# Kernel tuning notes

Hardware: AMD Instinct MI355X
Metric: run time of the kernel (lower is better)

Reference implementation:

```python
import jax, jax.numpy as jnp
import numpy as np

H = 64   # hidden_size
N = 128  # input_size (num nodes)
B = 64   # batch
T = 96   # seq_len
LN_EPS = 1e-5


def setup_inputs() -> dict:
    key = jax.random.key(0)
    ks = jax.random.split(key, 4)
    x = jax.random.normal(ks[0], (B, T, N), jnp.float32)
    # xavier_uniform-like scale for per-node gate weights [N, 1+H, 4H]
    lim = float(np.sqrt(6.0 / ((1 + H) + 4 * H)))
    w = jax.random.uniform(ks[1], (N, 1 + H, 4 * H), jnp.float32, -lim, lim)
    b = jnp.zeros((N, 4 * H), jnp.float32)
    ln_g = jnp.ones((H,), jnp.float32)
    ln_b = jnp.zeros((H,), jnp.float32)
    fc_w = jax.random.normal(ks[2], (1, H), jnp.float32) * (1.0 / np.sqrt(H))
    fc_b = jnp.zeros((1,), jnp.float32)
    return {"x": x, "w": w, "b": b, "ln_g": ln_g, "ln_b": ln_b,
            "fc_w": fc_w, "fc_b": fc_b}


def _crelu(z):
    return jnp.maximum(z.real, 0) + 1j * jnp.maximum(z.imag, 0)


def _csigmoid(z):
    # torch.sigmoid on complex: 1/(1+exp(-z))
    return 1.0 / (1.0 + jnp.exp(-z))


def _fc_att(x, pool_axes):
    # adaptive_avg_pool to 1 over pool_axes, (C)ReLU, sigmoid, rescale
    squeeze = jnp.mean(x, axis=pool_axes, keepdims=True)
    if jnp.iscomplexobj(x):
        exc = _crelu(squeeze)
        return x * _csigmoid(exc)
    exc = jnp.maximum(squeeze, 0)
    return x * jax.nn.sigmoid(exc)


def reference(x, w, b, ln_g, ln_b, fc_w, fc_b):
    Bb, Tt, Nn = x.shape
    h0 = jnp.zeros((Bb, Nn, H), x.dtype)
    c0 = jnp.zeros((Bb, Nn, H), x.dtype)

    def step(carry, x_t):  # x_t: [B, N]
        h, c = carry
        comb = jnp.concatenate([x_t[..., None], h], axis=-1)      # [B,N,1+H]
        gates = jnp.einsum('bni,nio->bno', comb, w) + b            # [B,N,4H]
        i_g, f_g, o_g, c_tilda = jnp.split(gates, 4, axis=-1)
        # NOTE: original cell does NOT apply tanh to c_tilda
        c_new = jax.nn.sigmoid(f_g) * c + jax.nn.sigmoid(i_g) * c_tilda
        h_new = jax.nn.sigmoid(o_g) * jnp.tanh(c_new)
        return (h_new, c_new), h_new

    _, hs = jax.lax.scan(step, (h0, c0), jnp.swapaxes(x, 0, 1))    # [T,B,N,H]
    lstm_out = jnp.sum(hs, axis=0)                                  # sum over time -> [B,N,H]

    # inter_op: FFT pairwise interaction over the node axis
    m = jnp.fft.rfft(lstm_out, axis=1, norm='ortho')                # [B,F,H] complex, F=N//2+1
    x_f = m[:, :, None, :] * m[:, None, :, :]                       # [B,F,F,H]
    x_f = _fc_att(x_f, (2, 3))
    x_f = jnp.sum(x_f, axis=1)                                      # [B,F,H]
    n_out = 2 * (x_f.shape[1] - 1)                                  # torch irfft default n
    feats = jnp.fft.irfft(x_f, n=n_out, axis=1, norm='ortho')       # [B,N,H] real
    feats = _fc_att(feats, (2,))
    out = jnp.sum(feats, axis=1)                                    # [B,H]

    # LayerNorm(H) -> Linear(H,1) -> sigmoid
    mu = jnp.mean(out, axis=-1, keepdims=True)
    var = jnp.var(out, axis=-1, keepdims=True)
    out = (out - mu) / jnp.sqrt(var + LN_EPS) * ln_g + ln_b
    out = out @ fc_w.T + fc_b                                       # [B,1]
    return jax.nn.sigmoid(out)
```

## Files before the change

kernel.cpp:

```cpp
#include <hip/hip_runtime.h>
#include <math.h>

#define T_STEPS 96
#define N_NODES 128
#define B_SZ 64
#define H_SZ 64

typedef __attribute__((ext_vector_type(8))) __bf16 bf16x8;
typedef __attribute__((ext_vector_type(4))) float f32x4;

__device__ __forceinline__ float rcp_fast(float x){ return __builtin_amdgcn_rcpf(x); }
__device__ __forceinline__ float exp2_fast(float x){ return __builtin_amdgcn_exp2f(x); }
__device__ __forceinline__ float sigm(float v){ return rcp_fast(1.0f + __expf(-v)); }

__global__ __launch_bounds__(512, 2) void lstm_kernel(
    const float* __restrict__ x, const float* __restrict__ w,
    const float* __restrict__ bias, float* __restrict__ yout)
{
  __shared__ __align__(16) unsigned short hb[2][16*72];
  __shared__ float xsl[T_STEPS*16];

  const int n   = blockIdx.x >> 2;
  const int bq  = blockIdx.x & 3;
  const int tid = threadIdx.x;
  const int wv  = tid >> 6;
  const int ln  = tid & 63;
  const int l15 = ln & 15;
  const int q   = ln >> 4;

  for (int i = tid; i < 2*16*72; i += 512) ((unsigned short*)hb)[i] = 0;
  for (int i = tid; i < T_STEPS*16; i += 512){
    int t2 = i >> 4, bl = i & 15;
    xsl[i] = x[(bq*16 + bl)*(T_STEPS*N_NODES) + t2*N_NODES + n];
  }

  const float LOG2E = 1.4426950408889634f;
  const float* wn = w + n*(65*256);

  bf16x8 aF[2][2];
  f32x4 w0t[2], bgt[2];
#pragma unroll
  for (int t = 0; t < 2; ++t){
    const int gA  = l15 & 3;
    const float scA = (gA < 3) ? LOG2E : 1.0f;
    const int colA = gA*64 + wv*8 + t*4 + (l15 >> 2);
#pragma unroll
    for (int ks = 0; ks < 2; ++ks)
#pragma unroll
      for (int j = 0; j < 8; ++j)
        aF[t][ks][j] = (__bf16)(wn[(1 + ks*32 + q*8 + j)*256 + colA] * scA);
#pragma unroll
    for (int r = 0; r < 4; ++r){
      const float sc = (r < 3) ? LOG2E : 1.0f;
      const int colD = r*64 + wv*8 + t*4 + q;
      w0t[t][r] = wn[colD] * sc;
      bgt[t][r] = bias[n*256 + colD] * sc;
    }
  }

  float cv[2]  = {0.f, 0.f};
  float hsv[2] = {0.f, 0.f};
  __syncthreads();

#pragma unroll 2
  for (int t = 0; t < T_STEPS; ++t){
    const unsigned short* cur = hb[t & 1];
    unsigned short*       nxt = (unsigned short*)hb[(t & 1) ^ 1];

    bf16x8 b0 = *(const bf16x8*)&cur[l15*72 +  0 + q*8];
    bf16x8 b1 = *(const bf16x8*)&cur[l15*72 + 32 + q*8];
    float xv = xsl[t*16 + l15];

    f32x4 acc[2];
#pragma unroll
    for (int tl = 0; tl < 2; ++tl){
      f32x4 a = w0t[tl]*xv + bgt[tl];
      a = __builtin_amdgcn_mfma_f32_16x16x32_bf16(aF[tl][0], b0, a, 0,0,0);
      a = __builtin_amdgcn_mfma_f32_16x16x32_bf16(aF[tl][1], b1, a, 0,0,0);
      acc[tl] = a;
    }

#pragma unroll
    for (int tl = 0; tl < 2; ++tl){
      float gi = acc[tl][0], gf = acc[tl][1], go = acc[tl][2], ct = acc[tl][3];
      float ei = exp2_fast(-gi), ef = exp2_fast(-gf);
      float pf = 1.0f + ef, pi = 1.0f + ei;
      float num = fmaf(cv[tl], ei, cv[tl]);
      num = fmaf(ct, pf, num);
      float cn = num * rcp_fast(pf*pi);
      cv[tl] = cn;
      float eo = exp2_fast(-go);
      float ea = fminf(cn*2.8853900817779268f, 126.0f);
      float ec = exp2_fast(ea);
      float hn = (ec - 1.0f) * rcp_fast((1.0f + eo)*(ec + 1.0f));
      hsv[tl] += hn;
      nxt[l15*72 + wv*8 + tl*4 + q] =
          __builtin_bit_cast(unsigned short, (__bf16)hn);
    }
    __syncthreads();
  }

#pragma unroll
  for (int tl = 0; tl < 2; ++tl)
    yout[((bq*16 + l15)*N_NODES + n)*H_SZ + wv*8 + tl*4 + q] = hsv[tl];
}

__global__ __launch_bounds__(256, 2) void dft_kernel(
    const float* __restrict__ y, float* __restrict__ Mout)
{
  __shared__ __align__(16) float ysl[128*20];
  __shared__ float twc[128], tws[128];
  const int b   = blockIdx.x >> 2;
  const int hg  = blockIdx.x & 3;
  const int tid = threadIdx.x;

  if (tid < 128){
    float ang = (float)((double)tid * 0.04908738521234052);
    twc[tid] = cosf(ang);
    tws[tid] = sinf(ang);
  }
  for (int i = tid; i < 128*16; i += 256){
    int nn = i >> 4, h = i & 15;
    ysl[nn*20 + h] = y[(b*N_NODES + nn)*H_SZ + hg*16 + h];
  }
  __syncthreads();

  for (int o = tid; o < 65*4; o += 256){
    int k  = o >> 2;
    int hq = o & 3;
    float re0=0,re1=0,re2=0,re3=0,im0=0,im1=0,im2=0,im3=0;
    for (int nn = 0; nn < 128; ++nn){
      float4 yv = *(const float4*)&ysl[nn*20 + hq*4];
      int j = (k*nn) & 127;
      float cc = twc[j], ss = tws[j];
      re0 = fmaf(yv.x, cc, re0); im0 = fmaf(yv.x, -ss, im0);
      re1 = fmaf(yv.y, cc, re1); im1 = fmaf(yv.y, -ss, im1);
      re2 = fmaf(yv.z, cc, re2); im2 = fmaf(yv.z, -ss, im2);
      re3 = fmaf(yv.w, cc, re3); im3 = fmaf(yv.w, -ss, im3);
    }
    const float s = 0.08838834764831845f;
    const int hb2 = hg*16 + hq*4;
    float* mre = Mout + ((b*2+0)*65 + k)*H_SZ + hb2;
    float* mim = Mout + ((b*2+1)*65 + k)*H_SZ + hb2;
    mre[0]=re0*s; mre[1]=re1*s; mre[2]=re2*s; mre[3]=re3*s;
    mim[0]=im0*s; mim[1]=im1*s; mim[2]=im2*s; mim[3]=im3*s;
  }
}

__global__ __launch_bounds__(256, 1) void post_kernel(
    const float* __restrict__ y, const float* __restrict__ Mws,
    const float* __restrict__ ln_g, const float* __restrict__ ln_b,
    const float* __restrict__ fc_w, const float* __restrict__ fc_b,
    float* __restrict__ out)
{
  __shared__ float ysh[128*65];
  __shared__ float Mre[65*65];
  __shared__ float Mim[65*65];
  __shared__ float twc[128], tws[128];
  __shared__ float Sre[64], Sim[64];
  __shared__ float gr[65], gi[65];
  __shared__ float Gre[64], Gim[64];
  __shared__ float att[128];
  __shared__ float PQ[65*2], AA[65*2];
  __shared__ float outv[64];

  const int b   = blockIdx.x;
  const int tid = threadIdx.x;

  if (tid < 128){
    float ang = (float)((double)tid * 0.04908738521234052);
    twc[tid] = cosf(ang);
    tws[tid] = sinf(ang);
  }
  for (int i = tid; i < 128*16; i += 256){
    int nn = i >> 4, h4 = (i & 15)*4;
    float4 v = *(const float4*)&y[(b*N_NODES + nn)*H_SZ + h4];
    ysh[nn*65 + h4+0] = v.x; ysh[nn*65 + h4+1] = v.y;
    ysh[nn*65 + h4+2] = v.z; ysh[nn*65 + h4+3] = v.w;
  }
  for (int i = tid; i < 65*16; i += 256){
    int k = i >> 4, h4 = (i & 15)*4;
    float4 vr = *(const float4*)&Mws[((b*2+0)*65 + k)*H_SZ + h4];
    float4 vi = *(const float4*)&Mws[((b*2+1)*65 + k)*H_SZ + h4];
    Mre[k*65 + h4+0] = vr.x; Mre[k*65 + h4+1] = vr.y;
    Mre[k*65 + h4+2] = vr.z; Mre[k*65 + h4+3] = vr.w;
    Mim[k*65 + h4+0] = vi.x; Mim[k*65 + h4+1] = vi.y;
    Mim[k*65 + h4+2] = vi.z; Mim[k*65 + h4+3] = vi.w;
  }
  __syncthreads();

  if (tid < 64){
    float sr=0, si=0;
    for (int k = 0; k < 65; ++k){ sr += Mre[k*65+tid]; si += Mim[k*65+tid]; }
    Sre[tid]=sr; Sim[tid]=si;
  }
  __syncthreads();

  if (tid < 65){
    float a=0, bb=0;
    for (int h = 0; h < 64; ++h){
      float mr = Mre[tid*65+h], mi = Mim[tid*65+h];
      a  += mr*Sre[h] - mi*Sim[h];
      bb += mr*Sim[h] + mi*Sre[h];
    }
    a  *= (1.0f/4160.0f);  bb *= (1.0f/4160.0f);
    a = fmaxf(a, 0.0f);    bb = fmaxf(bb, 0.0f);
    float t  = __expf(-a);
    float cb = cosf(bb), sb = sinf(bb);
    float dre = 1.0f + t*cb;
    float dim = t*sb;
    float nrm = rcp_fast(dre*dre + dim*dim);
    gr[tid] = dre*nrm;
    gi[tid] = dim*nrm;
  }
  __syncthreads();

  if (tid < 64){
    float grh=0, gih=0;
    for (int k = 0; k < 65; ++k){
      float mr = Mre[k*65+tid], mi = Mim[k*65+tid];
      float gk = gr[k], hk = gi[k];
      grh += gk*mr - hk*mi;
      gih += gk*mi + hk*mr;
    }
    Gre[tid]=grh; Gim[tid]=gih;
  }
  __syncthreads();

  if (tid < 65){
    float p=0, qq=0;
    for (int h = 0; h < 64; ++h){
      float gimh = Gim[h];
      p  += gimh * Mim[tid*65+h];
      qq += gimh * Mre[tid*65+h];
    }
    const float s2 = 2.0f*0.08838834764831845f;
    PQ[tid*2]   = p*s2;
    PQ[tid*2+1] = qq*s2;
  }
  __syncthreads();

  if (tid < 128){
    float u=0;
    for (int h = 0; h < 64; ++h) u += Gre[h]*ysh[tid*65+h];
    float v=0;
    for (int k = 1; k < 64; ++k){
      int j = (k*tid) & 127;
      v += PQ[k*2]*twc[j] + PQ[k*2+1]*tws[j];
    }
    float mean = (u - v)*(1.0f/64.0f);
    att[tid] = sigm(fmaxf(mean, 0.0f));
  }
  __syncthreads();

  if (tid < 65){
    float ac=0, as=0;
    for (int nn = 0; nn < 128; ++nn){
      int j = (tid*nn) & 127;
      float a2 = att[nn];
      ac = fmaf(a2, twc[j], ac);
      as = fmaf(a2, tws[j], as);
    }
    const float s2 = 2.0f*0.08838834764831845f;
    AA[tid*2]   = ac*s2;
    AA[tid*2+1] = as*s2;
  }
  __syncthreads();

  if (tid < 64){
    float wyh=0;
    for (int nn = 0; nn < 128; ++nn) wyh += att[nn]*ysh[nn*65+tid];
    float wHh=0;
    for (int k = 1; k < 64; ++k)
      wHh += Mim[k*65+tid]*AA[k*2] + Mre[k*65+tid]*AA[k*2+1];
    outv[tid] = Gre[tid]*wyh - Gim[tid]*wHh;
  }
  __syncthreads();

  if (tid < 64){
    float o = outv[tid];
    float s = o;
    for (int off = 32; off; off >>= 1) s += __shfl_xor(s, off, 64);
    float mu = s*(1.0f/64.0f);
    float d  = o - mu;
    float vv = d*d;
    for (int off = 32; off; off >>= 1) vv += __shfl_xor(vv, off, 64);
    float var = vv*(1.0f/64.0f);
    float zo = (d / sqrtf(var + 1e-5f))*ln_g[tid] + ln_b[tid];
    float z  = zo * fc_w[tid];
    for (int off = 32; off; off >>= 1) z += __shfl_xor(z, off, 64);
    if (tid == 0) out[b] = 1.0f/(1.0f + __expf(-(z + fc_b[0])));
  }
}

extern "C" void kernel_launch(void* const* d_in, const int* in_sizes, int n_in,
                              void* d_out, int out_size, void* d_ws, size_t ws_size,
                              hipStream_t stream) {
  (void)in_sizes; (void)n_in; (void)out_size; (void)ws_size;
  const float* x    = (const float*)d_in[0];
  const float* w    = (const float*)d_in[1];
  const float* bia  = (const float*)d_in[2];
  const float* ln_g = (const float*)d_in[3];
  const float* ln_b = (const float*)d_in[4];
  const float* fc_w = (const float*)d_in[5];
  const float* fc_b = (const float*)d_in[6];
  float* out = (float*)d_out;

  float* y = (float*)d_ws;
  float* M = y + (size_t)B_SZ*N_NODES*H_SZ;

  lstm_kernel<<<dim3(512), dim3(512), 0, stream>>>(x, w, bia, y);
  dft_kernel <<<dim3(256), dim3(256), 0, stream>>>(y, M);
  post_kernel<<<dim3(64),  dim3(256), 0, stream>>>(y, M, ln_g, ln_b, fc_w, fc_b, out);
}
```

Baseline: 172.1 us.

## Process 32 batch rows per LSTM block to halve grid and raise ILP

Each LSTM block now handles 32 batch rows (two 16-row MFMA sub-tiles) instead of 16, so the grid shrinks from 512 to 256 blocks. The two independent sub-tiles interleave their MFMAs and gate math within each timestep, which gives more instruction-level parallelism across the serial 96-step loop. It also halves the redundant per-block weight loads and conversions. The trade-off is fewer blocks, which on a GPU with many CUs may leave compute units idle, plus higher register and LDS use per block.

Result: no change. 175.3 us (+1.9%).

```diff
diff --git a/kernel.cpp b/kernel.cpp
--- a/kernel.cpp
+++ b/kernel.cpp
@@ -17,21 +17,21 @@
     const float* __restrict__ x, const float* __restrict__ w,
     const float* __restrict__ bias, float* __restrict__ yout)
 {
-  __shared__ __align__(16) unsigned short hb[2][16*72];
-  __shared__ float xsl[T_STEPS*16];
-
-  const int n   = blockIdx.x >> 2;
-  const int bq  = blockIdx.x & 3;
+  __shared__ __align__(16) unsigned short hb[2][32*72];
+  __shared__ float xsl[T_STEPS*32];
+
+  const int n   = blockIdx.x >> 1;
+  const int bh  = blockIdx.x & 1;
   const int tid = threadIdx.x;
   const int wv  = tid >> 6;
   const int ln  = tid & 63;
   const int l15 = ln & 15;
   const int q   = ln >> 4;
 
-  for (int i = tid; i < 2*16*72; i += 512) ((unsigned short*)hb)[i] = 0;
-  for (int i = tid; i < T_STEPS*16; i += 512){
-    int t2 = i >> 4, bl = i & 15;
-    xsl[i] = x[(bq*16 + bl)*(T_STEPS*N_NODES) + t2*N_NODES + n];
+  for (int i = tid; i < 2*32*72; i += 512) ((unsigned short*)hb)[i] = 0;
+  for (int i = tid; i < T_STEPS*32; i += 512){
+    int t2 = i >> 5, bl = i & 31;
+    xsl[i] = x[(bh*32 + bl)*(T_STEPS*N_NODES) + t2*N_NODES + n];
   }
 
   const float LOG2E = 1.4426950408889634f;
@@ -40,26 +40,26 @@
   bf16x8 aF[2][2];
   f32x4 w0t[2], bgt[2];
 #pragma unroll
-  for (int t = 0; t < 2; ++t){
+  for (int tl = 0; tl < 2; ++tl){
     const int gA  = l15 & 3;
     const float scA = (gA < 3) ? LOG2E : 1.0f;
-    const int colA = gA*64 + wv*8 + t*4 + (l15 >> 2);
+    const int colA = gA*64 + wv*8 + tl*4 + (l15 >> 2);
 #pragma unroll
     for (int ks = 0; ks < 2; ++ks)
 #pragma unroll
       for (int j = 0; j < 8; ++j)
-        aF[t][ks][j] = (__bf16)(wn[(1 + ks*32 + q*8 + j)*256 + colA] * scA);
+        aF[tl][ks][j] = (__bf16)(wn[(1 + ks*32 + q*8 + j)*256 + colA] * scA);
 #pragma unroll
     for (int r = 0; r < 4; ++r){
       const float sc = (r < 3) ? LOG2E : 1.0f;
-      const int colD = r*64 + wv*8 + t*4 + q;
-      w0t[t][r] = wn[colD] * sc;
-      bgt[t][r] = bias[n*256 + colD] * sc;
-    }
-  }
-
-  float cv[2]  = {0.f, 0.f};
-  float hsv[2] = {0.f, 0.f};
+      const int colD = r*64 + wv*8 + tl*4 + q;
+      w0t[tl][r] = wn[colD] * sc;
+      bgt[tl][r] = bias[n*256 + colD] * sc;
+    }
+  }
+
+  float cv[2][2]  = {{0.f,0.f},{0.f,0.f}};
+  float hsv[2][2] = {{0.f,0.f},{0.f,0.f}};
   __syncthreads();
 
 #pragma unroll 2
@@ -67,42 +67,55 @@
     const unsigned short* cur = hb[t & 1];
     unsigned short*       nxt = (unsigned short*)hb[(t & 1) ^ 1];
 
-    bf16x8 b0 = *(const bf16x8*)&cur[l15*72 +  0 + q*8];
-    bf16x8 b1 = *(const bf16x8*)&cur[l15*72 + 32 + q*8];
-    float xv = xsl[t*16 + l15];
-
-    f32x4 acc[2];
-#pragma unroll
-    for (int tl = 0; tl < 2; ++tl){
-      f32x4 a = w0t[tl]*xv + bgt[tl];
-      a = __builtin_amdgcn_mfma_f32_16x16x32_bf16(aF[tl][0], b0, a, 0,0,0);
-      a = __builtin_amdgcn_mfma_f32_16x16x32_bf16(aF[tl][1], b1, a, 0,0,0);
-      acc[tl] = a;
-    }
-
-#pragma unroll
-    for (int tl = 0; tl < 2; ++tl){
-      float gi = acc[tl][0], gf = acc[tl][1], go = acc[tl][2], ct = acc[tl][3];
-      float ei = exp2_fast(-gi), ef = exp2_fast(-gf);
-      float pf = 1.0f + ef, pi = 1.0f + ei;
-      float num = fmaf(cv[tl], ei, cv[tl]);
-      num = fmaf(ct, pf, num);
-      float cn = num * rcp_fast(pf*pi);
-      cv[tl] = cn;
-      float eo = exp2_fast(-go);
-      float ea = fminf(cn*2.8853900817779268f, 126.0f);
-      float ec = exp2_fast(ea);
-      float hn = (ec - 1.0f) * rcp_fast((1.0f + eo)*(ec + 1.0f));
-      hsv[tl] += hn;
-      nxt[l15*72 + wv*8 + tl*4 + q] =
-          __builtin_bit_cast(unsigned short, (__bf16)hn);
-    }
+    bf16x8 b0[2], b1[2];
+    float xv[2];
+#pragma unroll
+    for (int s = 0; s < 2; ++s){
+      const int bl = s*16 + l15;
+      b0[s] = *(const bf16x8*)&cur[bl*72 +  0 + q*8];
+      b1[s] = *(const bf16x8*)&cur[bl*72 + 32 + q*8];
+      xv[s] = xsl[t*32 + bl];
+    }
+
+    f32x4 acc[2][2];
+#pragma unroll
+    for (int s = 0; s < 2; ++s)
+#pragma unroll
+      for (int tl = 0; tl < 2; ++tl){
+        f32x4 a = w0t[tl]*xv[s] + bgt[tl];
+        a = __builtin_amdgcn_mfma_f32_16x16x32_bf16(aF[tl][0], b0[s], a, 0,0,0);
+        a = __builtin_amdgcn_mfma_f32_16x16x32_bf16(aF[tl][1], b1[s], a, 0,0,0);
+        acc[s][tl] = a;
+      }
+
+#pragma unroll
+    for (int s = 0; s < 2; ++s)
+#pragma unroll
+      for (int tl = 0; tl < 2; ++tl){
+        float gi = acc[s][tl][0], gf = acc[s][tl][1];
+        float go = acc[s][tl][2], ct = acc[s][tl][3];
+        float ei = exp2_fast(-gi), ef = exp2_fast(-gf);
+        float pf = 1.0f + ef, pi = 1.0f + ei;
+        float num = fmaf(cv[s][tl], ei, cv[s][tl]);
+        num = fmaf(ct, pf, num);
+        float cn = num * rcp_fast(pf*pi);
+        cv[s][tl] = cn;
+        float eo = exp2_fast(-go);
+        float ea = fminf(cn*2.8853900817779268f, 126.0f);
+        float ec = exp2_fast(ea);
+        float hn = (ec - 1.0f) * rcp_fast((1.0f + eo)*(ec + 1.0f));
+        hsv[s][tl] += hn;
+        nxt[(s*16 + l15)*72 + wv*8 + tl*4 + q] =
+            __builtin_bit_cast(unsigned short, (__bf16)hn);
+      }
     __syncthreads();
   }
 
 #pragma unroll
-  for (int tl = 0; tl < 2; ++tl)
-    yout[((bq*16 + l15)*N_NODES + n)*H_SZ + wv*8 + tl*4 + q] = hsv[tl];
+  for (int s = 0; s < 2; ++s)
+#pragma unroll
+    for (int tl = 0; tl < 2; ++tl)
+      yout[((bh*32 + s*16 + l15)*N_NODES + n)*H_SZ + wv*8 + tl*4 + q] = hsv[s][tl];
 }
 
 __global__ __launch_bounds__(256, 2) void dft_kernel(
@@ -309,7 +322,7 @@
   float* y = (float*)d_ws;
   float* M = y + (size_t)B_SZ*N_NODES*H_SZ;
 
-  lstm_kernel<<<dim3(512), dim3(512), 0, stream>>>(x, w, bia, y);
+  lstm_kernel<<<dim3(256), dim3(512), 0, stream>>>(x, w, bia, y);
   dft_kernel <<<dim3(256), dim3(256), 0, stream>>>(y, M);
   post_kernel<<<dim3(64),  dim3(256), 0, stream>>>(y, M, ln_g, ln_b, fc_w, fc_b, out);
 }
```
